# Kernel tuning notes

Measured on AMD Instinct MI355X. Metric: run time of the kernel, lower is better.

Reference implementation:

```python
import jax, jax.numpy as jnp
import numpy as np

N_NODES = 50000
N_EDGES = 320000
B = 4096          # subgraph batch: users/items/subg nodes
IN_N = 64         # in_nfeats
IN_E = 16         # in_efeats
OUT_E = 2 * IN_E  # out_edge_feats = in_efeats*2
H = 4             # num_heads
D = 64            # latent dim per layer (latent_dim=[64,64])
L = 2             # num EGAT layers


def setup_inputs() -> dict:
    key = jax.random.key(0)
    ks = iter(jax.random.split(key, 48))
    def nrm(shape, s=0.05):
        return jax.random.normal(next(ks), shape, dtype=jnp.float32) * s
    inp = {}
    inp['x'] = jax.random.normal(next(ks), (N_NODES, IN_N), dtype=jnp.float32)
    inp['efeat'] = jax.random.normal(next(ks), (N_EDGES, IN_E), dtype=jnp.float32)
    inp['efeat2'] = jax.random.normal(next(ks), (N_EDGES, IN_N), dtype=jnp.float32)
    inp['edge_mask'] = (jax.random.uniform(next(ks), (N_EDGES,)) > 0.1).astype(jnp.float32)
    inp['edge_mask2'] = (jax.random.uniform(next(ks), (N_EDGES,)) > 0.1).astype(jnp.float32)
    inp['src'] = jax.random.randint(next(ks), (N_EDGES,), 0, N_NODES, dtype=jnp.int32)
    inp['dst'] = jax.random.randint(next(ks), (N_EDGES,), 0, N_NODES, dtype=jnp.int32)
    inp['user_idx'] = jnp.arange(0, B, dtype=jnp.int32)          # ntype==0
    inp['item_idx'] = jnp.arange(B, 2 * B, dtype=jnp.int32)      # ntype==1
    inp['subg_idx'] = jnp.arange(2 * B, 3 * B, dtype=jnp.int32)  # ntype==-1
    # stacked per-layer EGAT params (layer dims identical since IN_N == D)
    inp['loc_wni'] = nrm((L, D, H * OUT_E))
    inp['loc_wnj'] = nrm((L, D, H * OUT_E))
    inp['loc_we'] = nrm((L, IN_E, H * OUT_E))
    inp['loc_attn'] = nrm((L, H, OUT_E))
    inp['loc_wnode'] = nrm((L, D, H * D))
    inp['agg1_w'] = nrm((L, H * D, D))
    inp['agg1_b'] = jnp.zeros((L, D), jnp.float32)
    inp['glob_wni'] = nrm((L, D, H * OUT_E))
    inp['glob_wnj'] = nrm((L, D, H * OUT_E))
    inp['glob_we'] = nrm((L, IN_N, H * OUT_E))
    inp['glob_attn'] = nrm((L, H, OUT_E))
    inp['glob_wnode'] = nrm((L, D, H * D))
    inp['agg2_w'] = nrm((L, H * D, D))
    inp['agg2_b'] = jnp.zeros((L, D), jnp.float32)
    inp['w1_ui'] = nrm((2 * L * D, 128))
    inp['b1_ui'] = jnp.zeros((128,), jnp.float32)
    inp['w1_sg'] = nrm((L * D, 128))
    inp['b1_sg'] = jnp.zeros((128,), jnp.float32)
    inp['w2_ui'] = nrm((128, 1))
    inp['b2_ui'] = jnp.zeros((1,), jnp.float32)
    inp['w2_sg'] = nrm((128, 1))
    inp['b2_sg'] = jnp.zeros((1,), jnp.float32)
    return inp


def _egat(x, e, norm, src, dst, wni, wnj, we, attn, wnode):
    # edge feature: f_ij = LeakyReLU(W_ni x_i + W_nj x_j + W_e e_ij), slope 0.2 (DGL EGATConv)
    f = (x @ wni)[src] + (x @ wnj)[dst] + e @ we            # (E, H*OUT_E)
    f = jax.nn.leaky_relu(f.reshape(-1, H, OUT_E), 0.2)
    scores = jnp.einsum('ehd,hd->eh', f, attn)              # (E, H)
    # edge softmax over incoming edges of each dst node
    m = jax.ops.segment_max(scores, dst, num_segments=N_NODES)
    m = jnp.where(jnp.isfinite(m), m, 0.0)
    ex = jnp.exp(scores - m[dst])
    denom = jax.ops.segment_sum(ex, dst, num_segments=N_NODES)
    a = ex / (denom[dst] + 1e-9)
    a = a * norm[:, None]                                    # per-edge norm (edge mask) weighting
    fn = (x @ wnode).reshape(-1, H, D)                       # (N, H, D)
    msg = fn[src] * a[:, :, None]                            # (E, H, D)
    out = jax.ops.segment_sum(msg, dst, num_segments=N_NODES)
    return out, a


def reference(x, efeat, efeat2, edge_mask, edge_mask2, src, dst, user_idx, item_idx, subg_idx,
              loc_wni, loc_wnj, loc_we, loc_attn, loc_wnode, agg1_w, agg1_b,
              glob_wni, glob_wnj, glob_we, glob_attn, glob_wnode, agg2_w, agg2_b,
              w1_ui, b1_ui, w1_sg, b1_sg, w2_ui, b2_ui, w2_sg, b2_sg):
    h = x
    ui_states, sg_states = [], []
    for l in range(L):
        out, _ = _egat(h, efeat, edge_mask, src, dst,
                       loc_wni[l], loc_wnj[l], loc_we[l], loc_attn[l], loc_wnode[l])
        h = jax.nn.elu(out.reshape(N_NODES, H * D) @ agg1_w[l] + agg1_b[l])
        ui_states.append(h)
        out, _ = _egat(h, efeat2, edge_mask2, src, dst,
                       glob_wni[l], glob_wnj[l], glob_we[l], glob_attn[l], glob_wnode[l])
        h = jax.nn.leaky_relu(out.reshape(N_NODES, H * D) @ agg2_w[l] + agg2_b[l], 0.01)
        sg_states.append(h)
    ui = jnp.concatenate(ui_states, axis=1)   # (N, L*D)
    sg = jnp.concatenate(sg_states, axis=1)   # (N, L*D)
    ui_x = jnp.concatenate([ui[user_idx], ui[item_idx]], axis=1)  # (B, 2*L*D)
    sg_x = sg[subg_idx]                                           # (B, L*D)
    ui_h = jax.nn.relu(ui_x @ w1_ui + b1_ui)  # dropout is identity in eval
    sg_h = jax.nn.relu(sg_x @ w1_sg + b1_sg)
    ui_out = jax.nn.sigmoid(ui_h @ w2_ui + b2_ui)[:, 0]
    sg_out = jax.nn.sigmoid(sg_h @ w2_sg + b2_sg)[:, 0]
    return (sg_out, ui_out)
```

## Files before the change

### kernel.cpp

```cpp
#include <hip/hip_runtime.h>
#include <math.h>

#define NN 50000
#define NE 320000
#define BATCH 4096

typedef __bf16 bf16x8 __attribute__((ext_vector_type(8)));
typedef float floatx4 __attribute__((ext_vector_type(4)));
typedef unsigned short ushort;
typedef unsigned int uint;

__device__ __forceinline__ float lrelu02(float x) { return x > 0.f ? x : 0.2f * x; }
__device__ __forceinline__ float b2f(ushort h) { return __uint_as_float(((uint)h) << 16); }
__device__ __forceinline__ float b2f_lo(uint u) { return __uint_as_float(u << 16); }
__device__ __forceinline__ float b2f_hi(uint u) { return __uint_as_float(u & 0xffff0000u); }
__device__ __forceinline__ ushort f2b(float x) {
    uint u = __float_as_uint(x);
    return (ushort)((u + 0x7fffu + ((u >> 16) & 1u)) >> 16);
}

__global__ __launch_bounds__(256) void score_gemm(
    const float* __restrict__ ef, int lda_ef, int ef_real, int ef_end, int KTOT,
    const ushort* __restrict__ Bt,
    const ushort* __restrict__ hb,
    const int* __restrict__ eidx, const int* __restrict__ srcv,
    const int* __restrict__ dstv,
    const float* __restrict__ attn, float* __restrict__ scv)
{
    __shared__ __align__(16) ushort As[64 * 32];
    __shared__ __align__(16) ushort Bs[128 * 32];
    const int tid = threadIdx.x;
    const int row0 = blockIdx.x << 6;
    const int w = tid >> 6, lane = tid & 63;
    const int quad = lane >> 4, l16 = lane & 15;
    const int arow = tid >> 2, c0 = (tid & 3) << 3;
    const int gr = row0 + arow;
    const int e_o = eidx[gr];
    const ushort* hs = hb + (size_t)srcv[gr] * 64;
    const ushort* hd = hb + (size_t)dstv[gr] * 64;

    floatx4 acc[8];
#pragma unroll
    for (int c = 0; c < 8; c++)
#pragma unroll
        for (int r = 0; r < 4; r++) acc[c][r] = 0.f;

    for (int kt = 0; kt < KTOT; kt += 32) {
        uint4 av = make_uint4(0u, 0u, 0u, 0u);
        if (kt < ef_end) {
            int col = kt + c0;
            if (col < ef_real) {
                const float* ap = ef + (size_t)e_o * lda_ef + col;
                float4 f0 = *(const float4*)ap;
                float4 f1 = *(const float4*)(ap + 4);
                av.x = (uint)f2b(f0.x) | ((uint)f2b(f0.y) << 16);
                av.y = (uint)f2b(f0.z) | ((uint)f2b(f0.w) << 16);
                av.z = (uint)f2b(f1.x) | ((uint)f2b(f1.y) << 16);
                av.w = (uint)f2b(f1.z) | ((uint)f2b(f1.w) << 16);
            }
        } else if (kt < ef_end + 64) {
            av = *(const uint4*)(hs + (kt - ef_end) + c0);
        } else {
            av = *(const uint4*)(hd + (kt - ef_end - 64) + c0);
        }
        *(uint4*)(As + arow * 32 + c0) = av;
#pragma unroll
        for (int it = 0; it < 2; it++) {
            int idx = it * 256 + tid;
            int bn = idx >> 2, bk = (idx & 3) << 3;
            *(uint4*)(Bs + bn * 32 + bk) = *(const uint4*)(Bt + (size_t)bn * KTOT + kt + bk);
        }
        __syncthreads();
        bf16x8 af = *(const bf16x8*)(As + (16 * w + l16) * 32 + quad * 8);
#pragma unroll
        for (int c = 0; c < 8; c++) {
            bf16x8 bfv = *(const bf16x8*)(Bs + (16 * c + l16) * 32 + quad * 8);
            acc[c] = __builtin_amdgcn_mfma_f32_16x16x32_bf16(af, bfv, acc[c], 0, 0, 0);
        }
        if (kt + 32 < KTOT) __syncthreads();
    }

    float av8[8];
#pragma unroll
    for (int c = 0; c < 8; c++)
        av8[c] = attn[(c >> 1) * 32 + (c & 1) * 16 + l16];
#pragma unroll
    for (int r = 0; r < 4; r++) {
        int orow = row0 + 16 * w + quad * 4 + r;
        float ph[4] = {0.f, 0.f, 0.f, 0.f};
#pragma unroll
        for (int c = 0; c < 8; c++) {
            float f = lrelu02(acc[c][r]);
            ph[c >> 1] = fmaf(f, av8[c], ph[c >> 1]);
        }
#pragma unroll
        for (int m = 1; m < 16; m <<= 1) {
#pragma unroll
            for (int h = 0; h < 4; h++) ph[h] += __shfl_xor(ph[h], m);
        }
        if (l16 == 0)
            *(float4*)(scv + (size_t)orow * 4) = make_float4(ph[0], ph[1], ph[2], ph[3]);
    }
}

__global__ __launch_bounds__(256) void gemm_agg(
    const ushort* __restrict__ A, int M,
    const ushort* __restrict__ Bt,
    const float* __restrict__ bias, int act,
    ushort* __restrict__ outb)
{
    __shared__ __align__(16) ushort As[64 * 32];
    __shared__ __align__(16) ushort Bs[64 * 32];
    const int tid = threadIdx.x;
    const int row0 = blockIdx.x << 6;
    const int w = tid >> 6, lane = tid & 63;
    const int quad = lane >> 4, l16 = lane & 15;
    const int arow = tid >> 2, c0 = (tid & 3) << 3;
    const int agrow = row0 + arow;

    floatx4 acc[4];
#pragma unroll
    for (int c = 0; c < 4; c++)
#pragma unroll
        for (int r = 0; r < 4; r++) acc[c][r] = 0.f;

    for (int kt = 0; kt < 256; kt += 32) {
        uint4 av = make_uint4(0u, 0u, 0u, 0u);
        if (agrow < M)
            av = *(const uint4*)(A + (size_t)agrow * 256 + kt + c0);
        *(uint4*)(As + arow * 32 + c0) = av;
        {
            int bn = tid >> 2, bk = (tid & 3) << 3;
            *(uint4*)(Bs + bn * 32 + bk) = *(const uint4*)(Bt + (size_t)bn * 256 + kt + bk);
        }
        __syncthreads();
        bf16x8 af = *(const bf16x8*)(As + (16 * w + l16) * 32 + quad * 8);
#pragma unroll
        for (int c = 0; c < 4; c++) {
            bf16x8 bfv = *(const bf16x8*)(Bs + (16 * c + l16) * 32 + quad * 8);
            acc[c] = __builtin_amdgcn_mfma_f32_16x16x32_bf16(af, bfv, acc[c], 0, 0, 0);
        }
        if (kt + 32 < 256) __syncthreads();
    }
#pragma unroll
    for (int r = 0; r < 4; r++) {
        int gr = row0 + 16 * w + quad * 4 + r;
        if (gr < M) {
#pragma unroll
            for (int c = 0; c < 4; c++) {
                int col = 16 * c + l16;
                float v = acc[c][r] + bias[col];
                if (act == 0) v = v > 0.f ? v : (__expf(v) - 1.f);
                else          v = v > 0.f ? v : 0.01f * v;
                outb[(size_t)gr * 64 + col] = f2b(v);
            }
        }
    }
}

__global__ void k_count(const int* __restrict__ dst, int* __restrict__ deg, int E)
{
    for (int i = blockIdx.x * blockDim.x + threadIdx.x; i < E; i += gridDim.x * blockDim.x)
        atomicAdd(&deg[dst[i]], 1);
}

__global__ __launch_bounds__(256) void scan_local(
    const int* __restrict__ deg, int* __restrict__ rowptr, int* __restrict__ partials, int N)
{
    __shared__ int sd[256];
    int tid = threadIdx.x;
    int i = blockIdx.x * 256 + tid;
    int v = (i < N) ? deg[i] : 0;
    sd[tid] = v; __syncthreads();
#pragma unroll
    for (int off = 1; off < 256; off <<= 1) {
        int t = (tid >= off) ? sd[tid - off] : 0;
        __syncthreads();
        sd[tid] += t;
        __syncthreads();
    }
    if (i < N) rowptr[i] = sd[tid] - v;
    if (tid == 255) partials[blockIdx.x] = sd[255];
}

__global__ __launch_bounds__(256) void scan_partials(int* __restrict__ partials, int nb)
{
    __shared__ int sd[256];
    int tid = threadIdx.x;
    int v = (tid < nb) ? partials[tid] : 0;
    sd[tid] = v; __syncthreads();
#pragma unroll
    for (int off = 1; off < 256; off <<= 1) {
        int t = (tid >= off) ? sd[tid - off] : 0;
        __syncthreads();
        sd[tid] += t;
        __syncthreads();
    }
    if (tid < nb) partials[tid] = sd[tid] - v;
}

__global__ void scan_add(int* __restrict__ rowptr, const int* __restrict__ partials, int N, int E)
{
    int i = blockIdx.x * 256 + threadIdx.x;
    if (i < N) rowptr[i] += partials[i >> 8];
    if (i == 0) rowptr[N] = E;
}

__global__ void k_scatter_perm(const int* __restrict__ dst, const int* __restrict__ rowptr,
                               int* __restrict__ cnt, const int* __restrict__ src,
                               const float* __restrict__ m1, const float* __restrict__ m2,
                               int* __restrict__ srcp, int* __restrict__ dstp,
                               int* __restrict__ eidx,
                               float* __restrict__ m1p, float* __restrict__ m2p, int E)
{
    for (int i = blockIdx.x * blockDim.x + threadIdx.x; i < E; i += gridDim.x * blockDim.x) {
        int d = dst[i];
        int p = rowptr[d] + atomicAdd(&cnt[d], 1);
        srcp[p] = src[i];
        dstp[p] = d;
        eidx[p] = i;
        m1p[p] = m1[i];
        m2p[p] = m2[i];
    }
}

__global__ void k_cvt(const float* __restrict__ in, ushort* __restrict__ out, int n)
{
    for (int i = blockIdx.x * blockDim.x + threadIdx.x; i < n; i += gridDim.x * blockDim.x)
        out[i] = f2b(in[i]);
}

__global__ void k_prep_score_all(const float* __restrict__ loc_we, const float* __restrict__ glob_we,
                                 const float* __restrict__ loc_wni, const float* __restrict__ glob_wni,
                                 const float* __restrict__ loc_wnj, const float* __restrict__ glob_wnj,
                                 ushort* __restrict__ B)
{
    int idx = blockIdx.x * 256 + threadIdx.x;
    if (idx >= 4 * 24576) return;
    int e = idx / 24576, rem = idx % 24576;
    int layer = e >> 1, gl = e & 1;
    int KTOT = gl ? 192 : 160;
    int ef_end = gl ? 64 : 32;
    int ef_real = gl ? 64 : 16;
    if (rem >= 128 * KTOT) return;
    int n = rem / KTOT, k = rem % KTOT;
    const float* we  = (gl ? glob_we  + layer * 64 * 128 : loc_we  + layer * 16 * 128);
    const float* wni = (gl ? glob_wni : loc_wni) + layer * 64 * 128;
    const float* wnj = (gl ? glob_wnj : loc_wnj) + layer * 64 * 128;
    float v;
    if (k < ef_end)            v = (k < ef_real) ? we[k * 128 + n] : 0.f;
    else if (k < ef_end + 64)  v = wni[(k - ef_end) * 128 + n];
    else                       v = wnj[(k - ef_end - 64) * 128 + n];
    B[e * 24576 + rem] = f2b(v);
}

__global__ void k_fold_all(const float* __restrict__ loc_wnode, const float* __restrict__ agg1_w,
                           const float* __restrict__ glob_wnode, const float* __restrict__ agg2_w,
                           ushort* __restrict__ B)
{
    int e = blockIdx.x >> 6;
    int idx = (blockIdx.x & 63) * 256 + threadIdx.x;
    int layer = e >> 1, gl = e & 1;
    const float* wnode = (gl ? glob_wnode : loc_wnode) + layer * 64 * 256;
    const float* aggw  = (gl ? agg2_w : agg1_w) + layer * 256 * 64;
    int j = idx >> 8, col = idx & 255;
    int h = col >> 6, ii = col & 63;
    float s = 0.f;
#pragma unroll 8
    for (int k = 0; k < 64; k++)
        s = fmaf(wnode[ii * 256 + h * 64 + k], aggw[(h * 64 + k) * 64 + j], s);
    B[e * 16384 + j * 256 + col] = f2b(s);
}

__global__ __launch_bounds__(256) void node_fused(
    const float* __restrict__ scv,
    const int* __restrict__ rowptr, const int* __restrict__ srcp,
    const float* __restrict__ maskp,
    const ushort* __restrict__ hsrc,
    ushort* __restrict__ zb)
{
    int tid = threadIdx.x;
    int n = (blockIdx.x << 4) | (tid >> 4);
    int sl = tid & 15;
    int beg = rowptr[n], end = rowptr[n + 1];
    float l0 = 0.f, l1 = 0.f, l2 = 0.f, l3 = 0.f;
    float acc[4][4] = {};
#pragma unroll 2
    for (int i = beg; i < end; i++) {
        float4 s4 = *(const float4*)(scv + (size_t)i * 4);
        float mk = maskp[i];
        int s = srcp[i];
        uint2 hvv = *(const uint2*)(hsrc + (size_t)s * 64 + sl * 4);
        float t0 = __expf(s4.x), t1 = __expf(s4.y), t2 = __expf(s4.z), t3 = __expf(s4.w);
        l0 += t0; l1 += t1; l2 += t2; l3 += t3;
        float a0 = t0 * mk, a1 = t1 * mk, a2 = t2 * mk, a3 = t3 * mk;
        float hv[4] = { b2f_lo(hvv.x), b2f_hi(hvv.x), b2f_lo(hvv.y), b2f_hi(hvv.y) };
#pragma unroll
        for (int c = 0; c < 4; c++) {
            acc[0][c] = fmaf(a0, hv[c], acc[0][c]);
            acc[1][c] = fmaf(a1, hv[c], acc[1][c]);
            acc[2][c] = fmaf(a2, hv[c], acc[2][c]);
            acc[3][c] = fmaf(a3, hv[c], acc[3][c]);
        }
    }
    float inv[4] = { 1.f / (l0 + 1e-9f), 1.f / (l1 + 1e-9f),
                     1.f / (l2 + 1e-9f), 1.f / (l3 + 1e-9f) };
#pragma unroll
    for (int h = 0; h < 4; h++) {
        uint2 o;
        o.x = (uint)f2b(acc[h][0] * inv[h]) | ((uint)f2b(acc[h][1] * inv[h]) << 16);
        o.y = (uint)f2b(acc[h][2] * inv[h]) | ((uint)f2b(acc[h][3] * inv[h]) << 16);
        *(uint2*)(zb + (size_t)n * 256 + h * 64 + sl * 4) = o;
    }
}

__global__ __launch_bounds__(256) void final_ui(
    const ushort* __restrict__ s0, const ushort* __restrict__ s1,
    const int* __restrict__ uidx, const int* __restrict__ iidx,
    const float* __restrict__ w1, const float* __restrict__ b1,
    const float* __restrict__ w2, const float* __restrict__ b2, float* __restrict__ out)
{
    __shared__ float xs[4][256];
    int tid = threadIdx.x, wid = tid >> 6, lane = tid & 63;
    int r = (blockIdx.x << 2) + wid;
    int u = uidx[r], it = iidx[r];
    xs[wid][lane]       = b2f(s0[(size_t)u * 64 + lane]);
    xs[wid][64 + lane]  = b2f(s1[(size_t)u * 64 + lane]);
    xs[wid][128 + lane] = b2f(s0[(size_t)it * 64 + lane]);
    xs[wid][192 + lane] = b2f(s1[(size_t)it * 64 + lane]);
    __syncthreads();
    int c = lane << 1;
    float a0 = b1[c], a1 = b1[c + 1];
    for (int k = 0; k < 256; k++) {
        float xv = xs[wid][k];
        float2 wv = *(const float2*)(w1 + (size_t)k * 128 + c);
        a0 = fmaf(xv, wv.x, a0);
        a1 = fmaf(xv, wv.y, a1);
    }
    a0 = fmaxf(a0, 0.f);
    a1 = fmaxf(a1, 0.f);
    float2 w2v = *(const float2*)(w2 + c);
    float p = a0 * w2v.x + a1 * w2v.y;
#pragma unroll
    for (int mm = 1; mm < 64; mm <<= 1) p += __shfl_xor(p, mm);
    if (lane == 0) out[r] = 1.f / (1.f + __expf(-(p + b2[0])));
}

__global__ __launch_bounds__(256) void final_sg(
    const ushort* __restrict__ s0, const ushort* __restrict__ s1,
    const int* __restrict__ gidx,
    const float* __restrict__ w1, const float* __restrict__ b1,
    const float* __restrict__ w2, const float* __restrict__ b2, float* __restrict__ out)
{
    __shared__ float xs[4][128];
    int tid = threadIdx.x, wid = tid >> 6, lane = tid & 63;
    int r = (blockIdx.x << 2) + wid;
    int n = gidx[r];
    xs[wid][lane]      = b2f(s0[(size_t)n * 64 + lane]);
    xs[wid][64 + lane] = b2f(s1[(size_t)n * 64 + lane]);
    __syncthreads();
    int c = lane << 1;
    float a0 = b1[c], a1 = b1[c + 1];
    for (int k = 0; k < 128; k++) {
        float xv = xs[wid][k];
        float2 wv = *(const float2*)(w1 + (size_t)k * 128 + c);
        a0 = fmaf(xv, wv.x, a0);
        a1 = fmaf(xv, wv.y, a1);
    }
    a0 = fmaxf(a0, 0.f);
    a1 = fmaxf(a1, 0.f);
    float2 w2v = *(const float2*)(w2 + c);
    float p = a0 * w2v.x + a1 * w2v.y;
#pragma unroll
    for (int mm = 1; mm < 64; mm <<= 1) p += __shfl_xor(p, mm);
    if (lane == 0) out[r] = 1.f / (1.f + __expf(-(p + b2[0])));
}

extern "C" void kernel_launch(void* const* d_in, const int* in_sizes, int n_in,
                              void* d_out, int out_size, void* d_ws, size_t ws_size,
                              hipStream_t stream)
{
    const float* x       = (const float*)d_in[0];
    const float* efeat   = (const float*)d_in[1];
    const float* efeat2  = (const float*)d_in[2];
    const float* mask1   = (const float*)d_in[3];
    const float* mask2   = (const float*)d_in[4];
    const int*   src     = (const int*)d_in[5];
    const int*   dst     = (const int*)d_in[6];
    const int*   uidx    = (const int*)d_in[7];
    const int*   iidx    = (const int*)d_in[8];
    const int*   gidx    = (const int*)d_in[9];
    const float* loc_wni = (const float*)d_in[10];
    const float* loc_wnj = (const float*)d_in[11];
    const float* loc_we  = (const float*)d_in[12];
    const float* loc_attn= (const float*)d_in[13];
    const float* loc_wnode=(const float*)d_in[14];
    const float* agg1_w  = (const float*)d_in[15];
    const float* agg1_b  = (const float*)d_in[16];
    const float* glob_wni= (const float*)d_in[17];
    const float* glob_wnj= (const float*)d_in[18];
    const float* glob_we = (const float*)d_in[19];
    const float* glob_attn=(const float*)d_in[20];
    const float* glob_wnode=(const float*)d_in[21];
    const float* agg2_w  = (const float*)d_in[22];
    const float* agg2_b  = (const float*)d_in[23];
    const float* w1_ui   = (const float*)d_in[24];
    const float* b1_ui   = (const float*)d_in[25];
    const float* w1_sg   = (const float*)d_in[26];
    const float* b1_sg   = (const float*)d_in[27];
    const float* w2_ui   = (const float*)d_in[28];
    const float* b2_ui   = (const float*)d_in[29];
    const float* w2_sg   = (const float*)d_in[30];
    const float* b2_sg   = (const float*)d_in[31];

    char* wsp = (char*)d_ws;
    auto carve = [&](size_t bytes) { char* p = wsp; wsp += (bytes + 255) & ~(size_t)255; return p; };
    ushort* zb    = (ushort*)carve((size_t)NN * 256 * 2);
    ushort* hb[5];
    for (int i = 0; i < 5; i++) hb[i] = (ushort*)carve((size_t)NN * 64 * 2);
    float*  scv   = (float*)carve((size_t)NE * 16);
    float*  m1p   = (float*)carve((size_t)NE * 4);
    float*  m2p   = (float*)carve((size_t)NE * 4);
    int*    srcp  = (int*)carve((size_t)NE * 4);
    int*    dstp  = (int*)carve((size_t)NE * 4);
    int*    eidx  = (int*)carve((size_t)NE * 4);
    ushort* Bsc   = (ushort*)carve(4 * 24576 * 2);
    ushort* Bfold = (ushort*)carve(4 * 16384 * 2);
    int* deg      = (int*)carve(NN * 4);
    int* rowptr   = (int*)carve((NN + 4) * 4);
    int* partials = (int*)carve(256 * 4);

    k_prep_score_all<<<384, 256, 0, stream>>>(loc_we, glob_we, loc_wni, glob_wni,
                                              loc_wnj, glob_wnj, Bsc);
    k_fold_all<<<256, 256, 0, stream>>>(loc_wnode, agg1_w, glob_wnode, agg2_w, Bfold);
    hipMemsetAsync(deg, 0, NN * sizeof(int), stream);
    k_count<<<1280, 256, 0, stream>>>(dst, deg, NE);
    scan_local<<<196, 256, 0, stream>>>(deg, rowptr, partials, NN);
    scan_partials<<<1, 256, 0, stream>>>(partials, 196);
    scan_add<<<196, 256, 0, stream>>>(rowptr, partials, NN, NE);
    hipMemsetAsync(deg, 0, NN * sizeof(int), stream);
    k_scatter_perm<<<1280, 256, 0, stream>>>(dst, rowptr, deg, src, mask1, mask2,
                                             srcp, dstp, eidx, m1p, m2p, NE);
    k_cvt<<<3200, 256, 0, stream>>>(x, hb[0], NN * 64);

    auto egat = [&](const ushort* hin, int e, const float* maskp, const float* attn,
                    const float* aggb, int act, ushort* hout) {
        int is_glob = e & 1;
        if (is_glob)
            score_gemm<<<5000, 256, 0, stream>>>(efeat2, 64, 64, 64, 192,
                                                 Bsc + e * 24576, hin,
                                                 eidx, srcp, dstp, attn, scv);
        else
            score_gemm<<<5000, 256, 0, stream>>>(efeat, 16, 16, 32, 160,
                                                 Bsc + e * 24576, hin,
                                                 eidx, srcp, dstp, attn, scv);
        node_fused<<<NN / 16, 256, 0, stream>>>(scv, rowptr, srcp, maskp, hin, zb);
        gemm_agg<<<782, 256, 0, stream>>>(zb, NN, Bfold + e * 16384, aggb, act, hout);
    };

    egat(hb[0], 0, m1p, loc_attn,        agg1_b,      0, hb[1]);
    egat(hb[1], 1, m2p, glob_attn,       agg2_b,      1, hb[2]);
    egat(hb[2], 2, m1p, loc_attn + 128,  agg1_b + 64, 0, hb[3]);
    egat(hb[3], 3, m2p, glob_attn + 128, agg2_b + 64, 1, hb[4]);

    float* out = (float*)d_out;
    final_sg<<<BATCH / 4, 256, 0, stream>>>(hb[2], hb[4], gidx, w1_sg, b1_sg, w2_sg, b2_sg, out);
    final_ui<<<BATCH / 4, 256, 0, stream>>>(hb[1], hb[3], uidx, iidx, w1_ui, b1_ui, w2_ui, b2_ui, out + BATCH);
}
```

Baseline: 627.9 us.

## Swap MFMA operands in score GEMM, preload weight fragments, sort edge buckets

The score kernel now keeps each lane's edge-feature and node rows in registers as the B operand. It loads the whole pre-swizzled weight matrix into LDS once per block, in MFMA fragment order, which removes the per-K-tile LDS staging and barriers. The weight prep kernel writes the fragment-ordered layout, and the epilogue is reworked to match the transposed accumulator layout. Edge buckets are now sorted by original edge index after the atomic scatter, which makes the permutation deterministic and gives more local access to efeat. This adds an insertion-sort kernel and a separate emit pass, and raises LDS use per block to up to 48KB.

```diff
diff --git a/kernel.cpp b/kernel.cpp
--- a/kernel.cpp
+++ b/kernel.cpp
@@ -19,25 +19,55 @@
     return (ushort)((u + 0x7fffu + ((u >> 16) & 1u)) >> 16);
 }
 
-__global__ __launch_bounds__(256) void score_gemm(
-    const float* __restrict__ ef, int lda_ef, int ef_real, int ef_end, int KTOT,
-    const ushort* __restrict__ Bt,
+template <int GLOB>
+__global__ __launch_bounds__(256) void score_frag(
+    const float* __restrict__ ef,
+    const ushort* __restrict__ Bfrag,
     const ushort* __restrict__ hb,
     const int* __restrict__ eidx, const int* __restrict__ srcv,
     const int* __restrict__ dstv,
     const float* __restrict__ attn, float* __restrict__ scv)
 {
-    __shared__ __align__(16) ushort As[64 * 32];
-    __shared__ __align__(16) ushort Bs[128 * 32];
+    constexpr int KTOT = GLOB ? 192 : 160;
+    constexpr int NR = KTOT / 32;
+    constexpr int EFR = GLOB ? 2 : 1;
+    constexpr int LDA = GLOB ? 64 : 16;
+    __shared__ __align__(16) ushort As[128 * KTOT];
     const int tid = threadIdx.x;
-    const int row0 = blockIdx.x << 6;
     const int w = tid >> 6, lane = tid & 63;
     const int quad = lane >> 4, l16 = lane & 15;
-    const int arow = tid >> 2, c0 = (tid & 3) << 3;
-    const int gr = row0 + arow;
-    const int e_o = eidx[gr];
-    const ushort* hs = hb + (size_t)srcv[gr] * 64;
-    const ushort* hd = hb + (size_t)dstv[gr] * 64;
+    const int row = (blockIdx.x << 6) + 16 * w + l16;
+
+    const int e_o = eidx[row];
+    const int s_n = srcv[row];
+    const int d_n = dstv[row];
+
+    bf16x8 bfr[NR];
+#pragma unroll
+    for (int rnd = 0; rnd < EFR; rnd++) {
+        uint4 av = make_uint4(0u, 0u, 0u, 0u);
+        int k0 = rnd * 32 + quad * 8;
+        if (GLOB || quad < 2) {
+            const float* ap = ef + (size_t)e_o * LDA + k0;
+            float4 f0 = *(const float4*)ap;
+            float4 f1 = *(const float4*)(ap + 4);
+            av.x = (uint)f2b(f0.x) | ((uint)f2b(f0.y) << 16);
+            av.y = (uint)f2b(f0.z) | ((uint)f2b(f0.w) << 16);
+            av.z = (uint)f2b(f1.x) | ((uint)f2b(f1.y) << 16);
+            av.w = (uint)f2b(f1.z) | ((uint)f2b(f1.w) << 16);
+        }
+        *(uint4*)&bfr[rnd] = av;
+    }
+#pragma unroll
+    for (int rr = 0; rr < 2; rr++)
+        bfr[EFR + rr] = *(const bf16x8*)(hb + (size_t)s_n * 64 + rr * 32 + quad * 8);
+#pragma unroll
+    for (int rr = 0; rr < 2; rr++)
+        bfr[EFR + 2 + rr] = *(const bf16x8*)(hb + (size_t)d_n * 64 + rr * 32 + quad * 8);
+
+    for (int i = tid; i < 128 * KTOT / 8; i += 256)
+        *(uint4*)(As + (size_t)i * 8) = *(const uint4*)(Bfrag + (size_t)i * 8);
+    __syncthreads();
 
     floatx4 acc[8];
 #pragma unroll
@@ -45,62 +75,33 @@
 #pragma unroll
         for (int r = 0; r < 4; r++) acc[c][r] = 0.f;
 
-    for (int kt = 0; kt < KTOT; kt += 32) {
-        uint4 av = make_uint4(0u, 0u, 0u, 0u);
-        if (kt < ef_end) {
-            int col = kt + c0;
-            if (col < ef_real) {
-                const float* ap = ef + (size_t)e_o * lda_ef + col;
-                float4 f0 = *(const float4*)ap;
-                float4 f1 = *(const float4*)(ap + 4);
-                av.x = (uint)f2b(f0.x) | ((uint)f2b(f0.y) << 16);
-                av.y = (uint)f2b(f0.z) | ((uint)f2b(f0.w) << 16);
-                av.z = (uint)f2b(f1.x) | ((uint)f2b(f1.y) << 16);
-                av.w = (uint)f2b(f1.z) | ((uint)f2b(f1.w) << 16);
-            }
-        } else if (kt < ef_end + 64) {
-            av = *(const uint4*)(hs + (kt - ef_end) + c0);
-        } else {
-            av = *(const uint4*)(hd + (kt - ef_end - 64) + c0);
-        }
-        *(uint4*)(As + arow * 32 + c0) = av;
-#pragma unroll
-        for (int it = 0; it < 2; it++) {
-            int idx = it * 256 + tid;
-            int bn = idx >> 2, bk = (idx & 3) << 3;
-            *(uint4*)(Bs + bn * 32 + bk) = *(const uint4*)(Bt + (size_t)bn * KTOT + kt + bk);
-        }
-        __syncthreads();
-        bf16x8 af = *(const bf16x8*)(As + (16 * w + l16) * 32 + quad * 8);
+#pragma unroll
+    for (int rnd = 0; rnd < NR; rnd++) {
 #pragma unroll
         for (int c = 0; c < 8; c++) {
-            bf16x8 bfv = *(const bf16x8*)(Bs + (16 * c + l16) * 32 + quad * 8);
-            acc[c] = __builtin_amdgcn_mfma_f32_16x16x32_bf16(af, bfv, acc[c], 0, 0, 0);
-        }
-        if (kt + 32 < KTOT) __syncthreads();
-    }
-
-    float av8[8];
-#pragma unroll
-    for (int c = 0; c < 8; c++)
-        av8[c] = attn[(c >> 1) * 32 + (c & 1) * 16 + l16];
-#pragma unroll
-    for (int r = 0; r < 4; r++) {
-        int orow = row0 + 16 * w + quad * 4 + r;
-        float ph[4] = {0.f, 0.f, 0.f, 0.f};
-#pragma unroll
-        for (int c = 0; c < 8; c++) {
-            float f = lrelu02(acc[c][r]);
-            ph[c >> 1] = fmaf(f, av8[c], ph[c >> 1]);
-        }
-#pragma unroll
-        for (int m = 1; m < 16; m <<= 1) {
-#pragma unroll
-            for (int h = 0; h < 4; h++) ph[h] += __shfl_xor(ph[h], m);
-        }
-        if (l16 == 0)
-            *(float4*)(scv + (size_t)orow * 4) = make_float4(ph[0], ph[1], ph[2], ph[3]);
-    }
+            bf16x8 afr = *(const bf16x8*)(As + ((size_t)(c * NR + rnd) * 64 + lane) * 8);
+            acc[c] = __builtin_amdgcn_mfma_f32_16x16x32_bf16(afr, bfr[rnd], acc[c], 0, 0, 0);
+        }
+    }
+
+    float ph[4] = {0.f, 0.f, 0.f, 0.f};
+#pragma unroll
+    for (int c = 0; c < 8; c++) {
+        int fbase = 16 * c + quad * 4;
+        float4 at4 = *(const float4*)(attn + fbase);
+        float v = lrelu02(acc[c][0]) * at4.x;
+        v = fmaf(lrelu02(acc[c][1]), at4.y, v);
+        v = fmaf(lrelu02(acc[c][2]), at4.z, v);
+        v = fmaf(lrelu02(acc[c][3]), at4.w, v);
+        ph[fbase >> 5] += v;
+    }
+#pragma unroll
+    for (int h = 0; h < 4; h++) {
+        ph[h] += __shfl_xor(ph[h], 16);
+        ph[h] += __shfl_xor(ph[h], 32);
+    }
+    if (quad == 0)
+        *(float4*)(scv + (size_t)row * 4) = make_float4(ph[0], ph[1], ph[2], ph[3]);
 }
 
 __global__ __launch_bounds__(256) void gemm_agg(
@@ -206,21 +207,42 @@
     if (i == 0) rowptr[N] = E;
 }
 
-__global__ void k_scatter_perm(const int* __restrict__ dst, const int* __restrict__ rowptr,
-                               int* __restrict__ cnt, const int* __restrict__ src,
-                               const float* __restrict__ m1, const float* __restrict__ m2,
-                               int* __restrict__ srcp, int* __restrict__ dstp,
-                               int* __restrict__ eidx,
-                               float* __restrict__ m1p, float* __restrict__ m2p, int E)
+__global__ void k_scatter(const int* __restrict__ dst, const int* __restrict__ rowptr,
+                          int* __restrict__ cnt, int* __restrict__ eidx, int E)
 {
     for (int i = blockIdx.x * blockDim.x + threadIdx.x; i < E; i += gridDim.x * blockDim.x) {
         int d = dst[i];
         int p = rowptr[d] + atomicAdd(&cnt[d], 1);
-        srcp[p] = src[i];
-        dstp[p] = d;
         eidx[p] = i;
-        m1p[p] = m1[i];
-        m2p[p] = m2[i];
+    }
+}
+
+__global__ void k_sort_buckets(const int* __restrict__ rowptr, int* __restrict__ eidx, int N)
+{
+    int n = blockIdx.x * blockDim.x + threadIdx.x;
+    if (n >= N) return;
+    int beg = rowptr[n], end = rowptr[n + 1];
+    for (int i = beg + 1; i < end; i++) {
+        int v = eidx[i];
+        int j = i - 1;
+        while (j >= beg && eidx[j] > v) { eidx[j + 1] = eidx[j]; j--; }
+        eidx[j + 1] = v;
+    }
+}
+
+__global__ void k_emit_perm(const int* __restrict__ eidx, const int* __restrict__ src,
+                            const int* __restrict__ dst,
+                            const float* __restrict__ m1, const float* __restrict__ m2,
+                            int* __restrict__ srcp, int* __restrict__ dstp,
+                            float* __restrict__ m1p, float* __restrict__ m2p, int E)
+{
+    int p = blockIdx.x * blockDim.x + threadIdx.x;
+    if (p < E) {
+        int e = eidx[p];
+        srcp[p] = src[e];
+        dstp[p] = dst[e];
+        m1p[p] = m1[e];
+        m2p[p] = m2[e];
     }
 }
 
@@ -240,17 +262,21 @@
     int e = idx / 24576, rem = idx % 24576;
     int layer = e >> 1, gl = e & 1;
     int KTOT = gl ? 192 : 160;
+    int NR = KTOT / 32;
     int ef_end = gl ? 64 : 32;
     int ef_real = gl ? 64 : 16;
     if (rem >= 128 * KTOT) return;
-    int n = rem / KTOT, k = rem % KTOT;
+    int j = rem & 7, lane = (rem >> 3) & 63, t = rem >> 9;
+    int c = t / NR, rnd = t % NR;
+    int m = 16 * c + (lane & 15);
+    int k = 32 * rnd + (lane >> 4) * 8 + j;
     const float* we  = (gl ? glob_we  + layer * 64 * 128 : loc_we  + layer * 16 * 128);
     const float* wni = (gl ? glob_wni : loc_wni) + layer * 64 * 128;
     const float* wnj = (gl ? glob_wnj : loc_wnj) + layer * 64 * 128;
     float v;
-    if (k < ef_end)            v = (k < ef_real) ? we[k * 128 + n] : 0.f;
-    else if (k < ef_end + 64)  v = wni[(k - ef_end) * 128 + n];
-    else                       v = wnj[(k - ef_end - 64) * 128 + n];
+    if (k < ef_end)            v = (k < ef_real) ? we[k * 128 + m] : 0.f;
+    else if (k < ef_end + 64)  v = wni[(k - ef_end) * 128 + m];
+    else                       v = wnj[(k - ef_end - 64) * 128 + m];
     B[e * 24576 + rem] = f2b(v);
 }
 
@@ -439,21 +465,21 @@
     scan_partials<<<1, 256, 0, stream>>>(partials, 196);
     scan_add<<<196, 256, 0, stream>>>(rowptr, partials, NN, NE);
     hipMemsetAsync(deg, 0, NN * sizeof(int), stream);
-    k_scatter_perm<<<1280, 256, 0, stream>>>(dst, rowptr, deg, src, mask1, mask2,
-                                             srcp, dstp, eidx, m1p, m2p, NE);
+    k_scatter<<<1280, 256, 0, stream>>>(dst, rowptr, deg, eidx, NE);
+    k_sort_buckets<<<196, 256, 0, stream>>>(rowptr, eidx, NN);
+    k_emit_perm<<<1250, 256, 0, stream>>>(eidx, src, dst, mask1, mask2,
+                                          srcp, dstp, m1p, m2p, NE);
     k_cvt<<<3200, 256, 0, stream>>>(x, hb[0], NN * 64);
 
     auto egat = [&](const ushort* hin, int e, const float* maskp, const float* attn,
                     const float* aggb, int act, ushort* hout) {
         int is_glob = e & 1;
         if (is_glob)
-            score_gemm<<<5000, 256, 0, stream>>>(efeat2, 64, 64, 64, 192,
-                                                 Bsc + e * 24576, hin,
-                                                 eidx, srcp, dstp, attn, scv);
+            score_frag<1><<<5000, 256, 0, stream>>>(efeat2, Bsc + e * 24576, hin,
+                                                    eidx, srcp, dstp, attn, scv);
         else
-            score_gemm<<<5000, 256, 0, stream>>>(efeat, 16, 16, 32, 160,
-                                                 Bsc + e * 24576, hin,
-                                                 eidx, srcp, dstp, attn, scv);
+            score_frag<0><<<5000, 256, 0, stream>>>(efeat, Bsc + e * 24576, hin,
+                                                    eidx, srcp, dstp, attn, scv);
         node_fused<<<NN / 16, 256, 0, stream>>>(scv, rowptr, srcp, maskp, hin, zb);
         gemm_agg<<<782, 256, 0, stream>>>(zb, NN, Bfold + e * 16384, aggb, act, hout);
     };
```

After: 593.3 us. -5.5%, faster.
